# Performance work log

Measured on AMD Instinct MI355X. Metric: run time of the kernel, lower is better.

The kernel has to match this reference:

```python
import jax, jax.numpy as jnp
import numpy as np

IN_DIM, DIM, H, L, B, N = 20, 128, 8, 3, 2, 192
DH = DIM // H
EPS = 1e-5


def _conv1d(x, w):
    # x: [b, Cin, n], w: [Cout, Cin, 3], pad=1
    return jax.lax.conv_general_dilated(x, w, (1,), [(1, 1)], dimension_numbers=('NCH', 'OIH', 'NCH'))


def _conv2d(x, w):
    # x: [b, Cin, n, n], w: [Cout, Cin, 3, 3], pad=1
    return jax.lax.conv_general_dilated(x, w, (1, 1), [(1, 1), (1, 1)], dimension_numbers=('NCHW', 'OIHW', 'NCHW'))


def _bn(x, g, b, axes):
    # BatchNorm in training mode (batch statistics, biased variance), channel axis = 1
    m = jnp.mean(x, axes, keepdims=True)
    v = jnp.var(x, axes, keepdims=True)
    sh = [1] * x.ndim
    sh[1] = -1
    return (x - m) / jnp.sqrt(v + EPS) * g.reshape(sh) + b.reshape(sh)


def _ln(x, g, b):
    m = jnp.mean(x, -1, keepdims=True)
    v = jnp.var(x, -1, keepdims=True)
    return (x - m) / jnp.sqrt(v + EPS) * g + b


def _seq2pair(c):
    # c: [b, C, n] -> [b, 2C, n, n]; first C channels constant over j, second C constant over i
    b, C, n = c.shape
    a = jnp.broadcast_to(c[:, :, :, None], (b, C, n, n))
    p = jnp.broadcast_to(c[:, :, None, :], (b, C, n, n))
    return jnp.concatenate([a, p], axis=1)


def _forward(seq, mask, conv1_w, conv2_w, ln_g, ln_b, c1d_w, bn1_g, bn1_b, c2d_w, bn2_g, bn2_b,
             wq_w, wq_b, wk_w, wk_b, wv_w, wv_b, wd_w, wd_b, wl_w, wl_b, fc_w, fc_b):
    b, n, _ = seq.shape
    s = seq.transpose(0, 2, 1)                    # [b, in_dim, n]
    x = _conv1d(s, conv1_w).transpose(0, 2, 1)    # [b, n, dim]
    c = _conv1d(s, conv2_w)                       # [b, dim, n]
    c2 = _seq2pair(c)                             # [b, 2*dim, n, n]
    scale = jnp.sqrt(jnp.asarray(DH, x.dtype))
    m4 = mask[:, None, None, :]                   # [b, 1, 1, n]
    for i in range(L):
        c = jax.nn.relu(_bn(_conv1d(c, c1d_w[i]), bn1_g[i], bn1_b[i], (0, 2)))
        x = _ln(x + c.transpose(0, 2, 1), ln_g[i], ln_b[i])
        c2 = c2 + _seq2pair(c)
        c2 = jax.nn.relu(_bn(_conv2d(c2, c2d_w[i]), bn2_g[i], bn2_b[i], (0, 2, 3)))
        dsym = c2 + c2.transpose(0, 1, 3, 2)      # symmetric pair features [b, 2*dim, n, n]
        gate = jax.nn.sigmoid(jnp.einsum('bcij,hc->bhij', dsym, wd_w[i]) + wd_b[i][None, :, None, None])
        heads = lambda y: y.reshape(b, n, H, DH).transpose(0, 2, 1, 3)
        q = heads(jax.nn.relu(x @ wq_w[i].T + wq_b[i]))
        k = heads(jax.nn.relu(x @ wk_w[i].T + wk_b[i]))
        v = heads(jax.nn.relu(x @ wv_w[i].T + wv_b[i]))
        a = jnp.einsum('bhid,bhjd->bhij', q, k) / scale
        e = jnp.exp(a - jnp.max(a, -1, keepdims=True)) * m4   # hand-rolled masked softmax
        attn = e / (jnp.sum(e, -1, keepdims=True) + 1e-6)
        attn = attn * gate                        # post-softmax multiplicative pair bias
        upd = jnp.einsum('bhij,bhjd->bhid', attn, v).transpose(0, 2, 1, 3).reshape(b, n, DIM)
        x = jax.nn.relu((x + upd) @ wl_w[i].T + wl_b[i])   # dropout = identity (eval)
    return jax.nn.relu(x @ fc_w.T + fc_b)


def setup_inputs():
    key = jax.random.key(0)
    ks = jax.random.split(key, 16)
    rn = lambda k, shape, s=0.05: jax.random.normal(k, shape, jnp.float32) * s
    C2 = 2 * DIM
    return {
        'seq': jax.random.normal(ks[0], (B, N, IN_DIM), jnp.float32),
        'mask': (jax.random.uniform(ks[1], (B, N)) > 0.1).astype(jnp.float32),
        'conv1_w': rn(ks[2], (DIM, IN_DIM, 3)),
        'conv2_w': rn(ks[3], (DIM, IN_DIM, 3)),
        'ln_g': jnp.ones((L, DIM), jnp.float32),
        'ln_b': jnp.zeros((L, DIM), jnp.float32),
        'c1d_w': rn(ks[4], (L, DIM, DIM, 3)),
        'bn1_g': jnp.ones((L, DIM), jnp.float32),
        'bn1_b': jnp.zeros((L, DIM), jnp.float32),
        'c2d_w': rn(ks[5], (L, C2, C2, 3, 3), 0.02),
        'bn2_g': jnp.ones((L, C2), jnp.float32),
        'bn2_b': jnp.zeros((L, C2), jnp.float32),
        'wq_w': rn(ks[6], (L, DIM, DIM)), 'wq_b': jnp.zeros((L, DIM), jnp.float32),
        'wk_w': rn(ks[7], (L, DIM, DIM)), 'wk_b': jnp.zeros((L, DIM), jnp.float32),
        'wv_w': rn(ks[8], (L, DIM, DIM)), 'wv_b': jnp.zeros((L, DIM), jnp.float32),
        'wd_w': rn(ks[9], (L, H, C2)), 'wd_b': jnp.zeros((L, H), jnp.float32),
        'wl_w': rn(ks[10], (L, DIM, DIM)), 'wl_b': jnp.zeros((L, DIM), jnp.float32),
        'fc_w': rn(ks[11], (DIM, DIM)), 'fc_b': jnp.zeros((DIM,), jnp.float32),
    }


def reference(seq, mask, conv1_w, conv2_w, ln_g, ln_b, c1d_w, bn1_g, bn1_b, c2d_w, bn2_g, bn2_b,
              wq_w, wq_b, wk_w, wk_b, wv_w, wv_b, wd_w, wd_b, wl_w, wl_b, fc_w, fc_b):
    return _forward(seq, mask, conv1_w, conv2_w, ln_g, ln_b, c1d_w, bn1_g, bn1_b, c2d_w, bn2_g, bn2_b,
                    wq_w, wq_b, wk_w, wk_b, wv_w, wv_b, wd_w, wd_b, wl_w, wl_b, fc_w, fc_b)
```

## Files before the change

kernel.cpp:

```cpp
#include <hip/hip_runtime.h>
#include <math.h>

#define IN_DIM 20
#define DIM 128
#define HH 8
#define LL 3
#define BB 2
#define NP 192
#define DHH 16
#define C2 256
#define NN (NP*NP)
#define EPS 1e-5f

#define PR 200
#define PC 224

typedef __bf16 bf16x8 __attribute__((ext_vector_type(8)));
typedef float  f32x16 __attribute__((ext_vector_type(16)));

union Pack8 { __bf16 h[8]; uint4 u; };

#define GLOAD16(gp, lp) \
  __builtin_amdgcn_global_load_lds((const __attribute__((address_space(1))) uint4*)(gp), \
                                   (__attribute__((address_space(3))) uint4*)(lp), 16, 0, 0)

__global__ void k_conv_init(const float* __restrict__ seq, const float* __restrict__ w1,
                            const float* __restrict__ w2, float* __restrict__ X,
                            float* __restrict__ Cc) {
  int t = blockIdx.x, b = blockIdx.y, oc = threadIdx.x;
  __shared__ float ss[3][IN_DIM];
  if (threadIdx.x < 3*IN_DIM) {
    int k = threadIdx.x / IN_DIM, ic = threadIdx.x % IN_DIM;
    int tt = t + k - 1;
    ss[k][ic] = (tt >= 0 && tt < NP) ? seq[(b*NP + tt)*IN_DIM + ic] : 0.f;
  }
  __syncthreads();
  float a1 = 0.f, a2 = 0.f;
  #pragma unroll
  for (int ic = 0; ic < IN_DIM; ic++) {
    #pragma unroll
    for (int k = 0; k < 3; k++) {
      float sv = ss[k][ic];
      a1 = fmaf(w1[(oc*IN_DIM + ic)*3 + k], sv, a1);
      a2 = fmaf(w2[(oc*IN_DIM + ic)*3 + k], sv, a2);
    }
  }
  X[(b*NP + t)*DIM + oc] = a1;
  Cc[(b*DIM + oc)*NP + t] = a2;
}

__global__ void k_conv1d_bn_relu(const float* __restrict__ cin, const float* __restrict__ w,
                                 const float* __restrict__ g, const float* __restrict__ bb,
                                 float* __restrict__ cout) {
  int oc = blockIdx.x;
  int t = threadIdx.x;
  float raw[BB];
  for (int b = 0; b < BB; b++) {
    float acc = 0.f;
    for (int ic = 0; ic < DIM; ic++) {
      const float* cr = cin + (b*DIM + ic)*NP;
      const float* wr = w + (oc*DIM + ic)*3;
      float lf = (t > 0)      ? cr[t-1] : 0.f;
      float mf = cr[t];
      float rf = (t < NP-1)   ? cr[t+1] : 0.f;
      acc = fmaf(lf, wr[0], acc);
      acc = fmaf(mf, wr[1], acc);
      acc = fmaf(rf, wr[2], acc);
    }
    raw[b] = acc;
  }
  __shared__ float sb[NP];
  sb[t] = raw[0] + raw[1];
  __syncthreads();
  for (int s = 128; s > 0; s >>= 1) {
    if (t < s && t + s < NP) sb[t] += sb[t + s];
    __syncthreads();
  }
  float mean = sb[0] / (float)(BB*NP);
  __syncthreads();
  sb[t] = raw[0]*raw[0] + raw[1]*raw[1];
  __syncthreads();
  for (int s = 128; s > 0; s >>= 1) {
    if (t < s && t + s < NP) sb[t] += sb[t + s];
    __syncthreads();
  }
  float var = sb[0] / (float)(BB*NP) - mean*mean;
  float rstd = rsqrtf(var + EPS);
  float gg = g[oc], bo = bb[oc];
  for (int b = 0; b < BB; b++)
    cout[(b*DIM + oc)*NP + t] = fmaxf((raw[b] - mean)*rstd*gg + bo, 0.f);
}

__global__ void k_wtrans(const float* __restrict__ wq, const float* __restrict__ wk,
                         const float* __restrict__ wv, const float* __restrict__ wl,
                         const float* __restrict__ fcw,
                         float* __restrict__ wqt, float* __restrict__ wkt,
                         float* __restrict__ wvt, float* __restrict__ wlt,
                         float* __restrict__ fct) {
  int m = blockIdx.y;
  const float* src; float* dst;
  if (m < 3)       { src = wq + (size_t)m*DIM*DIM;     dst = wqt + (size_t)m*DIM*DIM; }
  else if (m < 6)  { src = wk + (size_t)(m-3)*DIM*DIM; dst = wkt + (size_t)(m-3)*DIM*DIM; }
  else if (m < 9)  { src = wv + (size_t)(m-6)*DIM*DIM; dst = wvt + (size_t)(m-6)*DIM*DIM; }
  else if (m < 12) { src = wl + (size_t)(m-9)*DIM*DIM; dst = wlt + (size_t)(m-9)*DIM*DIM; }
  else             { src = fcw;                        dst = fct; }
  int tile = blockIdx.x;
  int ti = tile >> 2, tj = tile & 3;
  int r = threadIdx.x >> 3, c4 = threadIdx.x & 7;
  __shared__ float t[32][33];
  float4 v = *(const float4*)(src + (ti*32 + r)*DIM + tj*32 + c4*4);
  t[r][c4*4+0] = v.x; t[r][c4*4+1] = v.y; t[r][c4*4+2] = v.z; t[r][c4*4+3] = v.w;
  __syncthreads();
  float4 o;
  o.x = t[c4*4+0][r]; o.y = t[c4*4+1][r]; o.z = t[c4*4+2][r]; o.w = t[c4*4+3][r];
  *(float4*)(dst + (tj*32 + r)*DIM + ti*32 + c4*4) = o;
}

__global__ void k_lnqkv(float* __restrict__ X, const float* __restrict__ cc,
                        const float* __restrict__ g, const float* __restrict__ bb,
                        const float* __restrict__ wqt, const float* __restrict__ bq,
                        const float* __restrict__ wkt, const float* __restrict__ bk,
                        const float* __restrict__ wvt, const float* __restrict__ bv,
                        float* __restrict__ Q, float* __restrict__ K, float* __restrict__ V) {
  int t = blockIdx.x, b = blockIdx.y, d = threadIdx.x;
  __shared__ float sb[DIM];
  __shared__ float sy[DIM];
  float v = X[(b*NP + t)*DIM + d] + cc[(b*DIM + d)*NP + t];
  sb[d] = v; __syncthreads();
  for (int s = 64; s > 0; s >>= 1) { if (d < s) sb[d] += sb[d+s]; __syncthreads(); }
  float mean = sb[0] / (float)DIM;
  __syncthreads();
  float dv = v - mean;
  sb[d] = dv*dv; __syncthreads();
  for (int s = 64; s > 0; s >>= 1) { if (d < s) sb[d] += sb[d+s]; __syncthreads(); }
  float var = sb[0] / (float)DIM;
  float rstd = rsqrtf(var + EPS);
  float xn = dv * rstd * g[d] + bb[d];
  X[(b*NP + t)*DIM + d] = xn;
  sy[d] = xn;
  __syncthreads();
  float aq = bq[d], ak = bk[d], av = bv[d];
  for (int e = 0; e < DIM; e++) {
    float xv = sy[e];
    aq = fmaf(wqt[e*DIM + d], xv, aq);
    ak = fmaf(wkt[e*DIM + d], xv, ak);
    av = fmaf(wvt[e*DIM + d], xv, av);
  }
  int h = d >> 4, dh = d & 15;
  size_t o = ((size_t)(b*HH + h)*NP + t)*DHH + dh;
  Q[o] = fmaxf(aq, 0.f); K[o] = fmaxf(ak, 0.f); V[o] = fmaxf(av, 0.f);
}

__global__ void k_wprep(const float* __restrict__ w, __bf16* __restrict__ wtb) {
  int l = blockIdx.x / C2, oc = blockIdx.x % C2;
  int tid = threadIdx.x;
  __shared__ float swt[C2*9];
  const float4* wsrc = (const float4*)(w + ((size_t)(l*C2 + oc))*C2*9);
  for (int idx = tid; idx < 576; idx += 256) ((float4*)swt)[idx] = wsrc[idx];
  __syncthreads();
  for (int v = tid; v < 288; v += 256) {
    int chunk = v / 18, rem = v % 18;
    int kk = rem >> 1, kh = rem & 1;
    Pack8 p;
    #pragma unroll
    for (int e = 0; e < 8; e++)
      p.h[e] = (__bf16)swt[(chunk*16 + kh*8 + e)*9 + kk];
    size_t unit = ((((size_t)(l*16 + chunk)*9 + kk)*2 + kh)*256 + oc);
    ((uint4*)wtb)[unit] = p.u;
  }
}

__global__ void k_make_convin(const float* __restrict__ Cc, const float* __restrict__ CL0,
                              __bf16* __restrict__ inb, float* __restrict__ STATALL) {
  int idx = blockIdx.x*256 + threadIdx.x;
  if (blockIdx.x == 0) {
    for (int z = threadIdx.x; z < 3*2*C2; z += 256) STATALL[z] = 0.f;
  }
  int kh = idx & 1;
  int t = idx >> 1;
  int gcol = t % PC; int t2 = t / PC;
  int grow = t2 % PR; int t3 = t2 / PR;
  int chunk = t3 & 15; int b = t3 >> 4;
  int i = grow - 1, j = gcol - 8;
  Pack8 p;
  if ((unsigned)i < 192u && (unsigned)j < 192u) {
    #pragma unroll
    for (int e = 0; e < 8; e++) {
      int c = chunk*16 + kh*8 + e;
      float v;
      if (c < DIM) v = Cc[(b*DIM + c)*NP + i] + CL0[(b*DIM + c)*NP + i];
      else { int cc = c - DIM; v = Cc[(b*DIM + cc)*NP + j] + CL0[(b*DIM + cc)*NP + j]; }
      p.h[e] = (__bf16)v;
    }
  } else {
    #pragma unroll
    for (int e = 0; e < 8; e++) p.h[e] = (__bf16)0.f;
  }
  ((uint4*)inb)[idx] = p.u;
}

__global__ __launch_bounds__(256, 2)
void k_conv2d_mfma(const __bf16* __restrict__ inb,
                   const __bf16* __restrict__ wtb,
                   __bf16* __restrict__ rawb,
                   float* __restrict__ STAT2) {
  __shared__ __align__(16) uint4 sbuf[2*2176];
  int tid = threadIdx.x;
  int jt = blockIdx.x, it = blockIdx.y, zz = blockIdx.z;
  int b = zz >> 3, oct = zz & 7;
  int i0 = it*8, j0 = jt*64, oc0 = oct*32;
  int lane = tid & 63, wv = tid >> 6;
  int ln31 = lane & 31, khl = lane >> 5;

  const uint4* gW = (const uint4*)wtb;
  const uint4* gI = (const uint4*)inb;

  f32x16 acc[2][2];
  #pragma unroll
  for (int r = 0; r < 2; r++)
    #pragma unroll
    for (int n = 0; n < 2; n++)
      #pragma unroll
      for (int q = 0; q < 16; q++) acc[r][n][q] = 0.f;

  const uint4* gp[9];
  int lofs[9];
  int gstride[9];
  bool gvalid[9];
  #pragma unroll
  for (int t = 0; t < 9; t++) {
    int L = t*4 + wv;
    gvalid[t] = (L < 34);
    if (L < 9) {
      int u = L*64 + lane;
      int kkh = u >> 5;
      int ocl = u & 31;
      gp[t] = gW + (size_t)kkh*256 + oc0 + ocl;
      lofs[t] = u;
      gstride[t] = 4608;
    } else {
      int u = L*64 + lane - 576;
      int r = u / 160;
      int rem = u % 160;
      int kh = rem / 80;
      int c = rem % 80;
      gp[t] = gI + (((size_t)(b*16)*PR) + i0 + r)*PC*2 + (size_t)(j0 + c)*2 + kh;
      lofs[t] = 576 + u;
      gstride[t] = PR*PC*2;
    }
  }

  auto issue = [&](int buf) {
    uint4* lbase = sbuf + buf*2176;
    #pragma unroll
    for (int t = 0; t < 9; t++) {
      if (gvalid[t]) {
        GLOAD16(gp[t], lbase + lofs[t]);
        gp[t] += gstride[t];
      }
    }
  };

  issue(0);

  for (int chunk = 0; chunk < 16; ++chunk) {
    int buf = chunk & 1;
    __syncthreads();
    if (chunk < 15) issue(buf ^ 1);
    const __bf16* Wl = (const __bf16*)(sbuf + buf*2176);
    const __bf16* Il = (const __bf16*)(sbuf + buf*2176 + 576);
    #pragma unroll
    for (int kj = 0; kj < 3; kj++) {
      bf16x8 bfr[4][2];
      #pragma unroll
      for (int rr = 0; rr < 4; rr++) {
        int r = wv*2 + rr;
        #pragma unroll
        for (int ch = 0; ch < 2; ch++) {
          int c = ch*32 + ln31 + kj + 7;
          bfr[rr][ch] = *(const bf16x8*)(Il + ((r*2 + khl)*80 + c)*8);
        }
      }
      #pragma unroll
      for (int ki = 0; ki < 3; ki++) {
        int kk = ki*3 + kj;
        bf16x8 a = *(const bf16x8*)(Wl + ((kk*2 + khl)*32 + ln31)*8);
        #pragma unroll
        for (int row = 0; row < 2; row++)
          #pragma unroll
          for (int ch = 0; ch < 2; ch++)
            acc[row][ch] = __builtin_amdgcn_mfma_f32_32x32x16_bf16(a, bfr[row + ki][ch], acc[row][ch], 0, 0, 0);
      }
    }
  }

  __syncthreads();
  float* trAll = (float*)sbuf;
  float* tr = trAll + wv*(32*33);
  float* sstat = trAll + 4*32*33;
  if (tid < 64) sstat[tid] = 0.f;
  __syncthreads();

  #pragma unroll
  for (int reg = 0; reg < 16; reg++) {
    float v00 = acc[0][0][reg], v01 = acc[0][1][reg];
    float v10 = acc[1][0][reg], v11 = acc[1][1][reg];
    float s = v00 + v01 + v10 + v11;
    float s2 = v00*v00 + v01*v01 + v10*v10 + v11*v11;
    #pragma unroll
    for (int msk = 1; msk <= 16; msk <<= 1) { s += __shfl_xor(s, msk); s2 += __shfl_xor(s2, msk); }
    if (ln31 == 0) {
      int oc_l = (reg & 3) + 8*(reg >> 2) + 4*khl;
      atomicAdd(&sstat[oc_l], s);
      atomicAdd(&sstat[32 + oc_l], s2);
    }
  }

  int Gb = oc0 >> 3;
  uint4* RAWu = (uint4*)rawb;
  #pragma unroll
  for (int row = 0; row < 2; row++) {
    int i = i0 + wv*2 + row;
    #pragma unroll
    for (int ch = 0; ch < 2; ch++) {
      #pragma unroll
      for (int reg = 0; reg < 16; reg++) {
        int r = (reg & 3) + 8*(reg >> 2) + 4*khl;
        tr[r*33 + ln31] = acc[row][ch][reg];
      }
      __builtin_amdgcn_s_waitcnt(0);
      #pragma unroll
      for (int gs = 0; gs < 2; gs++) {
        int g = khl + gs*2;
        Pack8 p;
        #pragma unroll
        for (int e = 0; e < 8; e++) p.h[e] = (__bf16)tr[(g*8 + e)*33 + ln31];
        RAWu[((size_t)(b*32 + Gb + g)*192 + i)*192 + j0 + ch*32 + ln31] = p.u;
      }
      __builtin_amdgcn_s_waitcnt(0);
    }
  }

  __syncthreads();
  if (tid < 32) {
    atomicAdd(&STAT2[oc0 + tid], sstat[tid]);
    atomicAdd(&STAT2[C2 + oc0 + tid], sstat[32 + tid]);
  }
}

template<int WRITE_NEXT>
__global__ void k_bn2_norm_gate(const __bf16* __restrict__ rawb, const float* __restrict__ STAT2,
                                const float* __restrict__ g, const float* __restrict__ bb,
                                const float* __restrict__ wd, const float* __restrict__ CLn,
                                __bf16* __restrict__ inb_next, float* __restrict__ tg) {
  int i = blockIdx.x, b = blockIdx.y, j = threadIdx.x;
  __shared__ float sscale[C2], sshift[C2], swd[HH*C2];
  const float inv = 1.f / (float)(BB*NN);
  for (int c = j; c < C2; c += 192) {
    float mean = STAT2[c] * inv;
    float var  = STAT2[C2 + c] * inv - mean*mean;
    float rstd = rsqrtf(var + EPS);
    float sc = rstd * g[c];
    sscale[c] = sc;
    sshift[c] = bb[c] - mean*sc;
  }
  for (int idx = j; idx < HH*C2; idx += 192) swd[idx] = wd[idx];
  __syncthreads();
  float gacc[HH] = {};
  const uint4* RAWu = (const uint4*)rawb;
  for (int cu = 0; cu < 32; cu++) {
    Pack8 pr; pr.u = RAWu[((size_t)(b*32 + cu)*NP + i)*NP + j];
    Pack8 p;
    #pragma unroll
    for (int e = 0; e < 8; e++) {
      int c = cu*8 + e;
      float v = (float)pr.h[e];
      v = fmaxf(fmaf(v, sscale[c], sshift[c]), 0.f);
      if (WRITE_NEXT) {
        float nv = v + ((c < DIM) ? CLn[(b*DIM + c)*NP + i] : CLn[(b*DIM + c - DIM)*NP + j]);
        p.h[e] = (__bf16)nv;
      }
      #pragma unroll
      for (int h = 0; h < HH; h++) gacc[h] = fmaf(v, swd[h*C2 + c], gacc[h]);
    }
    if (WRITE_NEXT) {
      size_t unit = ((((size_t)(b*16 + (cu>>1))*PR + (i+1))*PC + (j+8))*2 + (cu&1));
      ((uint4*)inb_next)[unit] = p.u;
    }
  }
  for (int h = 0; h < HH; h++)
    tg[((size_t)(b*HH + h)*NP + i)*NP + j] = gacc[h];
}

__global__ void k_gate(const float* __restrict__ tg, const float* __restrict__ wdb,
                       float* __restrict__ gate) {
  int tile = blockIdx.x;
  int hb = blockIdx.y;
  int b = hb >> 3, h = hb & 7;
  size_t bh = (size_t)(b*HH + h);
  int ti = tile / 6, tj = tile % 6;
  int r = threadIdx.x >> 3, c4 = threadIdx.x & 7;
  __shared__ float tB[32][33];
  const float* base = tg + bh*NN;
  float4 vb = *(const float4*)(base + (tj*32 + r)*NP + ti*32 + c4*4);
  tB[r][c4*4+0] = vb.x; tB[r][c4*4+1] = vb.y; tB[r][c4*4+2] = vb.z; tB[r][c4*4+3] = vb.w;
  __syncthreads();
  float4 va = *(const float4*)(base + (ti*32 + r)*NP + tj*32 + c4*4);
  float bias = wdb[h];
  float4 o;
  o.x = 1.f / (1.f + expf(-(va.x + tB[c4*4+0][r] + bias)));
  o.y = 1.f / (1.f + expf(-(va.y + tB[c4*4+1][r] + bias)));
  o.z = 1.f / (1.f + expf(-(va.z + tB[c4*4+2][r] + bias)));
  o.w = 1.f / (1.f + expf(-(va.w + tB[c4*4+3][r] + bias)));
  *(float4*)(gate + bh*NN + (ti*32 + r)*NP + tj*32 + c4*4) = o;
}

template<int MODE>
__global__ __launch_bounds__(192)
void k_attnx(const float* __restrict__ Q, const float* __restrict__ K,
             const float* __restrict__ V, const float* __restrict__ gate,
             const float* __restrict__ mask,
             float* __restrict__ X,
             const float* __restrict__ wlt, const float* __restrict__ bl,
             const float* __restrict__ ccn,
             const float* __restrict__ lng, const float* __restrict__ lnb,
             const float* __restrict__ wqt, const float* __restrict__ bq,
             const float* __restrict__ wkt, const float* __restrict__ bk,
             const float* __restrict__ wvt, const float* __restrict__ bv,
             float* __restrict__ Qn, float* __restrict__ Kn, float* __restrict__ Vn,
             const float* __restrict__ fct, const float* __restrict__ fb,
             float* __restrict__ out) {
  int i = blockIdx.x, b = blockIdx.y, j = threadIdx.x;
  int lane = j & 63, wvv = j >> 6;
  __shared__ float sq[DIM];
  __shared__ float sattn[HH][NP];
  __shared__ float supd[DIM];
  __shared__ float sy[DIM];
  __shared__ float sredm[HH][3];
  __shared__ float sreds[HH][3];
  __shared__ float sred[3];
  float mk = mask[b*NP + j];

  if (j < DIM) {
    int h = j >> 4, d = j & 15;
    sq[j] = Q[(((size_t)(b*HH + h))*NP + i)*DHH + d];
  }
  __syncthreads();

  float a[HH], gt[HH];
  #pragma unroll
  for (int h = 0; h < HH; h++) {
    size_t bh = (size_t)(b*HH + h);
    const float4* kr = (const float4*)(K + (bh*NP + j)*DHH);
    const float4* qr = (const float4*)(sq + h*DHH);
    float acc = 0.f;
    #pragma unroll
    for (int q4 = 0; q4 < 4; q4++) {
      float4 qv = qr[q4], kv = kr[q4];
      acc = fmaf(qv.x, kv.x, acc); acc = fmaf(qv.y, kv.y, acc);
      acc = fmaf(qv.z, kv.z, acc); acc = fmaf(qv.w, kv.w, acc);
    }
    a[h] = acc * 0.25f;
    gt[h] = gate[(bh*NP + i)*NP + j];
  }
  #pragma unroll
  for (int h = 0; h < HH; h++) {
    float m = a[h];
    #pragma unroll
    for (int s = 32; s > 0; s >>= 1) m = fmaxf(m, __shfl_xor(m, s));
    if (lane == 0) sredm[h][wvv] = m;
  }
  __syncthreads();
  float e[HH];
  #pragma unroll
  for (int h = 0; h < HH; h++) {
    float amax = fmaxf(fmaxf(sredm[h][0], sredm[h][1]), sredm[h][2]);
    e[h] = expf(a[h] - amax) * mk;
    float ss = e[h];
    #pragma unroll
    for (int s = 32; s > 0; s >>= 1) ss += __shfl_xor(ss, s);
    if (lane == 0) sreds[h][wvv] = ss;
  }
  __syncthreads();
  #pragma unroll
  for (int h = 0; h < HH; h++) {
    float denom = sreds[h][0] + sreds[h][1] + sreds[h][2] + 1e-6f;
    sattn[h][j] = (e[h] / denom) * gt[h];
  }
  __syncthreads();

  if (j < DIM) {
    int h = j >> 4, d = j & 15;
    size_t bh = (size_t)(b*HH + h);
    float acc = 0.f;
    for (int jj = 0; jj < NP; jj++)
      acc = fmaf(sattn[h][jj], V[(bh*NP + jj)*DHH + d], acc);
    supd[h*DHH + d] = acc;
  }
  __syncthreads();

  size_t o = (size_t)(b*NP + i)*DIM;
  if (j < DIM) sy[j] = X[o + j] + supd[j];
  __syncthreads();
  float xr = 0.f;
  if (j < DIM) {
    float acc = bl[j];
    for (int ee = 0; ee < DIM; ee++) acc = fmaf(wlt[ee*DIM + j], sy[ee], acc);
    xr = fmaxf(acc, 0.f);
  }
  __syncthreads();

  if (MODE == 0) {
    float v = 0.f;
    if (j < DIM) v = xr + ccn[(b*DIM + j)*NP + i];
    float s = (j < DIM) ? v : 0.f;
    #pragma unroll
    for (int m = 32; m > 0; m >>= 1) s += __shfl_xor(s, m);
    if (lane == 0 && wvv < 2) sred[wvv] = s;
    __syncthreads();
    float mean = (sred[0] + sred[1]) * (1.f/128.f);
    float dv = v - mean;
    float q = (j < DIM) ? dv*dv : 0.f;
    #pragma unroll
    for (int m = 32; m > 0; m >>= 1) q += __shfl_xor(q, m);
    __syncthreads();
    if (lane == 0 && wvv < 2) sred[wvv] = q;
    __syncthreads();
    float var = (sred[0] + sred[1]) * (1.f/128.f);
    float rstd = rsqrtf(var + EPS);
    if (j < DIM) {
      float xn = dv * rstd * lng[j] + lnb[j];
      X[o + j] = xn;
      sy[j] = xn;
    }
    __syncthreads();
    if (j < DIM) {
      float aq = bq[j], ak = bk[j], av = bv[j];
      for (int ee = 0; ee < DIM; ee++) {
        float xv = sy[ee];
        aq = fmaf(wqt[ee*DIM + j], xv, aq);
        ak = fmaf(wkt[ee*DIM + j], xv, ak);
        av = fmaf(wvt[ee*DIM + j], xv, av);
      }
      int h = j >> 4, dh = j & 15;
      size_t oo = ((size_t)(b*HH + h)*NP + i)*DHH + dh;
      Qn[oo] = fmaxf(aq, 0.f); Kn[oo] = fmaxf(ak, 0.f); Vn[oo] = fmaxf(av, 0.f);
    }
  } else {
    if (j < DIM) sy[j] = xr;
    __syncthreads();
    if (j < DIM) {
      float acc = fb[j];
      for (int ee = 0; ee < DIM; ee++) acc = fmaf(fct[ee*DIM + j], sy[ee], acc);
      out[o + j] = fmaxf(acc, 0.f);
    }
  }
}

extern "C" void kernel_launch(void* const* d_in, const int* in_sizes, int n_in,
                              void* d_out, int out_size, void* d_ws, size_t ws_size,
                              hipStream_t stream) {
  const float* seq     = (const float*)d_in[0];
  const float* mask    = (const float*)d_in[1];
  const float* conv1_w = (const float*)d_in[2];
  const float* conv2_w = (const float*)d_in[3];
  const float* ln_g    = (const float*)d_in[4];
  const float* ln_b    = (const float*)d_in[5];
  const float* c1d_w   = (const float*)d_in[6];
  const float* bn1_g   = (const float*)d_in[7];
  const float* bn1_b   = (const float*)d_in[8];
  const float* c2d_w   = (const float*)d_in[9];
  const float* bn2_g   = (const float*)d_in[10];
  const float* bn2_b   = (const float*)d_in[11];
  const float* wq_w    = (const float*)d_in[12];
  const float* wq_b    = (const float*)d_in[13];
  const float* wk_w    = (const float*)d_in[14];
  const float* wk_b    = (const float*)d_in[15];
  const float* wv_w    = (const float*)d_in[16];
  const float* wv_b    = (const float*)d_in[17];
  const float* wd_w    = (const float*)d_in[18];
  const float* wd_b    = (const float*)d_in[19];
  const float* wl_w    = (const float*)d_in[20];
  const float* wl_b    = (const float*)d_in[21];
  const float* fc_w    = (const float*)d_in[22];
  const float* fc_b    = (const float*)d_in[23];
  float* out = (float*)d_out;

  float* ws = (float*)d_ws;
  float* X    = ws; ws += BB*NP*DIM;
  float* Cc   = ws; ws += BB*DIM*NP;
  float* CL0  = ws; ws += BB*DIM*NP;
  float* CL1  = ws; ws += BB*DIM*NP;
  float* CL2  = ws; ws += BB*DIM*NP;
  float* Q0   = ws; ws += BB*NP*DIM;
  float* K0   = ws; ws += BB*NP*DIM;
  float* V0   = ws; ws += BB*NP*DIM;
  float* Q1   = ws; ws += BB*NP*DIM;
  float* K1   = ws; ws += BB*NP*DIM;
  float* V1   = ws; ws += BB*NP*DIM;
  float* TG   = ws; ws += (size_t)BB*HH*NN;
  float* GATE = ws; ws += (size_t)BB*HH*NN;
  float* WQT  = ws; ws += (size_t)LL*DIM*DIM;
  float* WKT  = ws; ws += (size_t)LL*DIM*DIM;
  float* WVT  = ws; ws += (size_t)LL*DIM*DIM;
  float* WLT  = ws; ws += (size_t)LL*DIM*DIM;
  float* FCT  = ws; ws += (size_t)DIM*DIM;
  float* STATALL = ws; ws += 3*2*C2;
  __bf16* RAW = (__bf16*)ws; ws += (size_t)BB*C2*NN/2;
  __bf16* INB = (__bf16*)ws; ws += (size_t)BB*16*PR*PC*2*16/4;
  __bf16* WTB = (__bf16*)ws; ws += (size_t)LL*C2*C2*9/2;

  k_wtrans<<<dim3(16, 13), 256, 0, stream>>>(wq_w, wk_w, wv_w, wl_w, fc_w,
                                             WQT, WKT, WVT, WLT, FCT);
  k_wprep<<<LL*C2, 256, 0, stream>>>(c2d_w, WTB);
  k_conv_init<<<dim3(NP, BB), DIM, 0, stream>>>(seq, conv1_w, conv2_w, X, Cc);
  k_conv1d_bn_relu<<<DIM, NP, 0, stream>>>(Cc,  c1d_w + 0*(size_t)DIM*DIM*3, bn1_g + 0*DIM, bn1_b + 0*DIM, CL0);
  k_conv1d_bn_relu<<<DIM, NP, 0, stream>>>(CL0, c1d_w + 1*(size_t)DIM*DIM*3, bn1_g + 1*DIM, bn1_b + 1*DIM, CL1);
  k_conv1d_bn_relu<<<DIM, NP, 0, stream>>>(CL1, c1d_w + 2*(size_t)DIM*DIM*3, bn1_g + 2*DIM, bn1_b + 2*DIM, CL2);
  k_make_convin<<<(BB*16*PR*PC*2)/256, 256, 0, stream>>>(Cc, CL0, INB, STATALL);
  k_lnqkv<<<dim3(NP, BB), DIM, 0, stream>>>(X, CL0, ln_g, ln_b,
                                            WQT, wq_b, WKT, wk_b, WVT, wv_b, Q0, K0, V0);

  k_conv2d_mfma<<<dim3(3, 24, 16), 256, 0, stream>>>(INB, WTB + 0*(size_t)16*9*2*256*8, RAW, STATALL + 0*2*C2);
  k_bn2_norm_gate<1><<<dim3(NP, BB), NP, 0, stream>>>(RAW, STATALL + 0*2*C2, bn2_g + 0*C2, bn2_b + 0*C2,
                                                      wd_w + 0*(size_t)HH*C2, CL1, INB, TG);
  k_gate<<<dim3(36, 16), 256, 0, stream>>>(TG, wd_b + 0*HH, GATE);
  k_attnx<0><<<dim3(NP, BB), NP, 0, stream>>>(Q0, K0, V0, GATE, mask, X,
                                              WLT + 0*(size_t)DIM*DIM, wl_b + 0*DIM,
                                              CL1, ln_g + 1*DIM, ln_b + 1*DIM,
                                              WQT + 1*(size_t)DIM*DIM, wq_b + 1*DIM,
                                              WKT + 1*(size_t)DIM*DIM, wk_b + 1*DIM,
                                              WVT + 1*(size_t)DIM*DIM, wv_b + 1*DIM,
                                              Q1, K1, V1, nullptr, nullptr, nullptr);
  k_conv2d_mfma<<<dim3(3, 24, 16), 256, 0, stream>>>(INB, WTB + 1*(size_t)16*9*2*256*8, RAW, STATALL + 1*2*C2);
  k_bn2_norm_gate<1><<<dim3(NP, BB), NP, 0, stream>>>(RAW, STATALL + 1*2*C2, bn2_g + 1*C2, bn2_b + 1*C2,
                                                      wd_w + 1*(size_t)HH*C2, CL2, INB, TG);
  k_gate<<<dim3(36, 16), 256, 0, stream>>>(TG, wd_b + 1*HH, GATE);
  k_attnx<0><<<dim3(NP, BB), NP, 0, stream>>>(Q1, K1, V1, GATE, mask, X,
                                              WLT + 1*(size_t)DIM*DIM, wl_b + 1*DIM,
                                              CL2, ln_g + 2*DIM, ln_b + 2*DIM,
                                              WQT + 2*(size_t)DIM*DIM, wq_b + 2*DIM,
                                              WKT + 2*(size_t)DIM*DIM, wk_b + 2*DIM,
                                              WVT + 2*(size_t)DIM*DIM, wv_b + 2*DIM,
                                              Q0, K0, V0, nullptr, nullptr, nullptr);
  k_conv2d_mfma<<<dim3(3, 24, 16), 256, 0, stream>>>(INB, WTB + 2*(size_t)16*9*2*256*8, RAW, STATALL + 2*2*C2);
  k_bn2_norm_gate<0><<<dim3(NP, BB), NP, 0, stream>>>(RAW, STATALL + 2*2*C2, bn2_g + 2*C2, bn2_b + 2*C2,
                                                      wd_w + 2*(size_t)HH*C2, nullptr, nullptr, TG);
  k_gate<<<dim3(36, 16), 256, 0, stream>>>(TG, wd_b + 2*HH, GATE);
  k_attnx<1><<<dim3(NP, BB), NP, 0, stream>>>(Q0, K0, V0, GATE, mask, X,
                                              WLT + 2*(size_t)DIM*DIM, wl_b + 2*DIM,
                                              nullptr, nullptr, nullptr,
                                              nullptr, nullptr, nullptr, nullptr, nullptr, nullptr,
                                              nullptr, nullptr, nullptr,
                                              FCT, fc_b, out);
}
```

Baseline: 680.1 us.

## Split per-thread work across more threads in conv1d, bn2-gate and attention kernels

Raises block sizes for three small kernels and splits each thread's serial loops. The 1-D conv gets 768 threads (batch × input-channel halves) with a merged mean/variance reduction. The BN2+gate pass splits its channel loop in half and combines through shared memory. The attention kernel splits heads, PV sums and the linear layers across 384 threads. The aim is to cut the long serial dependency chains and idle lanes in these latency-bound kernels, at the cost of extra shared-memory reductions and barriers.

```diff
diff --git a/kernel.cpp b/kernel.cpp
--- a/kernel.cpp
+++ b/kernel.cpp
@@ -49,46 +49,44 @@
   Cc[(b*DIM + oc)*NP + t] = a2;
 }
 
-__global__ void k_conv1d_bn_relu(const float* __restrict__ cin, const float* __restrict__ w,
-                                 const float* __restrict__ g, const float* __restrict__ bb,
-                                 float* __restrict__ cout) {
+__global__ __launch_bounds__(768)
+void k_conv1d_bn_relu(const float* __restrict__ cin, const float* __restrict__ w,
+                      const float* __restrict__ g, const float* __restrict__ bb,
+                      float* __restrict__ cout) {
   int oc = blockIdx.x;
-  int t = threadIdx.x;
-  float raw[BB];
-  for (int b = 0; b < BB; b++) {
-    float acc = 0.f;
-    for (int ic = 0; ic < DIM; ic++) {
-      const float* cr = cin + (b*DIM + ic)*NP;
-      const float* wr = w + (oc*DIM + ic)*3;
-      float lf = (t > 0)      ? cr[t-1] : 0.f;
-      float mf = cr[t];
-      float rf = (t < NP-1)   ? cr[t+1] : 0.f;
-      acc = fmaf(lf, wr[0], acc);
-      acc = fmaf(mf, wr[1], acc);
-      acc = fmaf(rf, wr[2], acc);
-    }
-    raw[b] = acc;
-  }
-  __shared__ float sb[NP];
-  sb[t] = raw[0] + raw[1];
-  __syncthreads();
-  for (int s = 128; s > 0; s >>= 1) {
-    if (t < s && t + s < NP) sb[t] += sb[t + s];
+  int tid = threadIdx.x;
+  int t = tid % NP;
+  int sub = tid / NP;
+  int b = sub & 1, ih = sub >> 1;
+  float acc = 0.f;
+  for (int ic = ih*64; ic < ih*64 + 64; ic++) {
+    const float* cr = cin + (b*DIM + ic)*NP;
+    const float* wr = w + (oc*DIM + ic)*3;
+    float lf = (t > 0)      ? cr[t-1] : 0.f;
+    float mf = cr[t];
+    float rf = (t < NP-1)   ? cr[t+1] : 0.f;
+    acc = fmaf(lf, wr[0], acc);
+    acc = fmaf(mf, wr[1], acc);
+    acc = fmaf(rf, wr[2], acc);
+  }
+  __shared__ float sp[4][NP];
+  __shared__ float sb[768];
+  sp[sub][t] = acc;
+  __syncthreads();
+  float raw = sp[b][t] + sp[2 + b][t];
+  sb[tid] = (sub < 2) ? raw : raw * raw;
+  __syncthreads();
+  for (int s = 192; s >= 3; s >>= 1) {
+    if (tid < s) sb[tid] += sb[tid + s];
+    int u = tid - 384;
+    if (u >= 0 && u < s) sb[tid] += sb[tid + s];
     __syncthreads();
   }
-  float mean = sb[0] / (float)(BB*NP);
-  __syncthreads();
-  sb[t] = raw[0]*raw[0] + raw[1]*raw[1];
-  __syncthreads();
-  for (int s = 128; s > 0; s >>= 1) {
-    if (t < s && t + s < NP) sb[t] += sb[t + s];
-    __syncthreads();
-  }
-  float var = sb[0] / (float)(BB*NP) - mean*mean;
+  float mean = (sb[0] + sb[1] + sb[2]) / 384.f;
+  float var  = (sb[384] + sb[385] + sb[386]) / 384.f - mean*mean;
   float rstd = rsqrtf(var + EPS);
-  float gg = g[oc], bo = bb[oc];
-  for (int b = 0; b < BB; b++)
-    cout[(b*DIM + oc)*NP + t] = fmaxf((raw[b] - mean)*rstd*gg + bo, 0.f);
+  if (sub < 2)
+    cout[(b*DIM + oc)*NP + t] = fmaxf((raw - mean)*rstd*g[oc] + bb[oc], 0.f);
 }
 
 __global__ void k_wtrans(const float* __restrict__ wq, const float* __restrict__ wk,
@@ -349,14 +347,18 @@
 }
 
 template<int WRITE_NEXT>
-__global__ void k_bn2_norm_gate(const __bf16* __restrict__ rawb, const float* __restrict__ STAT2,
-                                const float* __restrict__ g, const float* __restrict__ bb,
-                                const float* __restrict__ wd, const float* __restrict__ CLn,
-                                __bf16* __restrict__ inb_next, float* __restrict__ tg) {
-  int i = blockIdx.x, b = blockIdx.y, j = threadIdx.x;
+__global__ __launch_bounds__(384)
+void k_bn2_norm_gate(const __bf16* __restrict__ rawb, const float* __restrict__ STAT2,
+                     const float* __restrict__ g, const float* __restrict__ bb,
+                     const float* __restrict__ wd, const float* __restrict__ CLn,
+                     __bf16* __restrict__ inb_next, float* __restrict__ tg) {
+  int i = blockIdx.x, b = blockIdx.y;
+  int tid = threadIdx.x;
+  int j = tid % 192, half = tid / 192;
   __shared__ float sscale[C2], sshift[C2], swd[HH*C2];
+  __shared__ float sg[2][HH][192];
   const float inv = 1.f / (float)(BB*NN);
-  for (int c = j; c < C2; c += 192) {
+  for (int c = tid; c < C2; c += 384) {
     float mean = STAT2[c] * inv;
     float var  = STAT2[C2 + c] * inv - mean*mean;
     float rstd = rsqrtf(var + EPS);
@@ -364,11 +366,11 @@
     sscale[c] = sc;
     sshift[c] = bb[c] - mean*sc;
   }
-  for (int idx = j; idx < HH*C2; idx += 192) swd[idx] = wd[idx];
+  for (int idx = tid; idx < HH*C2; idx += 384) swd[idx] = wd[idx];
   __syncthreads();
   float gacc[HH] = {};
   const uint4* RAWu = (const uint4*)rawb;
-  for (int cu = 0; cu < 32; cu++) {
+  for (int cu = half*16; cu < half*16 + 16; cu++) {
     Pack8 pr; pr.u = RAWu[((size_t)(b*32 + cu)*NP + i)*NP + j];
     Pack8 p;
     #pragma unroll
@@ -388,8 +390,14 @@
       ((uint4*)inb_next)[unit] = p.u;
     }
   }
-  for (int h = 0; h < HH; h++)
-    tg[((size_t)(b*HH + h)*NP + i)*NP + j] = gacc[h];
+  #pragma unroll
+  for (int h = 0; h < HH; h++) sg[half][h][j] = gacc[h];
+  __syncthreads();
+  if (half == 0) {
+    #pragma unroll
+    for (int h = 0; h < HH; h++)
+      tg[((size_t)(b*HH + h)*NP + i)*NP + j] = sg[0][h][j] + sg[1][h][j];
+  }
 }
 
 __global__ void k_gate(const float* __restrict__ tg, const float* __restrict__ wdb,
@@ -416,7 +424,7 @@
 }
 
 template<int MODE>
-__global__ __launch_bounds__(192)
+__global__ __launch_bounds__(384)
 void k_attnx(const float* __restrict__ Q, const float* __restrict__ K,
              const float* __restrict__ V, const float* __restrict__ gate,
              const float* __restrict__ mask,
@@ -430,26 +438,31 @@
              float* __restrict__ Qn, float* __restrict__ Kn, float* __restrict__ Vn,
              const float* __restrict__ fct, const float* __restrict__ fb,
              float* __restrict__ out) {
-  int i = blockIdx.x, b = blockIdx.y, j = threadIdx.x;
-  int lane = j & 63, wvv = j >> 6;
+  int i = blockIdx.x, b = blockIdx.y;
+  int tid = threadIdx.x;
+  int j = tid % 192, half = tid / 192;
+  int lane = tid & 63, wave = tid >> 6;
   __shared__ float sq[DIM];
   __shared__ float sattn[HH][NP];
+  __shared__ float spv[3][DIM];
   __shared__ float supd[DIM];
   __shared__ float sy[DIM];
+  __shared__ float sxp[3][DIM];
   __shared__ float sredm[HH][3];
   __shared__ float sreds[HH][3];
-  __shared__ float sred[3];
+  __shared__ float sred[2];
   float mk = mask[b*NP + j];
 
-  if (j < DIM) {
-    int h = j >> 4, d = j & 15;
-    sq[j] = Q[(((size_t)(b*HH + h))*NP + i)*DHH + d];
-  }
-  __syncthreads();
-
-  float a[HH], gt[HH];
-  #pragma unroll
-  for (int h = 0; h < HH; h++) {
+  if (tid < DIM) {
+    int h = tid >> 4, d = tid & 15;
+    sq[tid] = Q[(((size_t)(b*HH + h))*NP + i)*DHH + d];
+  }
+  __syncthreads();
+
+  float a[4], gt[4];
+  #pragma unroll
+  for (int hh = 0; hh < 4; hh++) {
+    int h = half*4 + hh;
     size_t bh = (size_t)(b*HH + h);
     const float4* kr = (const float4*)(K + (bh*NP + j)*DHH);
     const float4* qr = (const float4*)(sq + h*DHH);
@@ -460,100 +473,115 @@
       acc = fmaf(qv.x, kv.x, acc); acc = fmaf(qv.y, kv.y, acc);
       acc = fmaf(qv.z, kv.z, acc); acc = fmaf(qv.w, kv.w, acc);
     }
-    a[h] = acc * 0.25f;
-    gt[h] = gate[(bh*NP + i)*NP + j];
-  }
-  #pragma unroll
-  for (int h = 0; h < HH; h++) {
-    float m = a[h];
+    a[hh] = acc * 0.25f;
+    gt[hh] = gate[(bh*NP + i)*NP + j];
+  }
+  #pragma unroll
+  for (int hh = 0; hh < 4; hh++) {
+    int h = half*4 + hh;
+    float m = a[hh];
     #pragma unroll
     for (int s = 32; s > 0; s >>= 1) m = fmaxf(m, __shfl_xor(m, s));
-    if (lane == 0) sredm[h][wvv] = m;
-  }
-  __syncthreads();
-  float e[HH];
-  #pragma unroll
-  for (int h = 0; h < HH; h++) {
+    if (lane == 0) sredm[h][wave % 3] = m;
+  }
+  __syncthreads();
+  float e[4];
+  #pragma unroll
+  for (int hh = 0; hh < 4; hh++) {
+    int h = half*4 + hh;
     float amax = fmaxf(fmaxf(sredm[h][0], sredm[h][1]), sredm[h][2]);
-    e[h] = expf(a[h] - amax) * mk;
-    float ss = e[h];
+    e[hh] = expf(a[hh] - amax) * mk;
+    float ss = e[hh];
     #pragma unroll
     for (int s = 32; s > 0; s >>= 1) ss += __shfl_xor(ss, s);
-    if (lane == 0) sreds[h][wvv] = ss;
-  }
-  __syncthreads();
-  #pragma unroll
-  for (int h = 0; h < HH; h++) {
+    if (lane == 0) sreds[h][wave % 3] = ss;
+  }
+  __syncthreads();
+  #pragma unroll
+  for (int hh = 0; hh < 4; hh++) {
+    int h = half*4 + hh;
     float denom = sreds[h][0] + sreds[h][1] + sreds[h][2] + 1e-6f;
-    sattn[h][j] = (e[h] / denom) * gt[h];
-  }
-  __syncthreads();
-
-  if (j < DIM) {
-    int h = j >> 4, d = j & 15;
-    size_t bh = (size_t)(b*HH + h);
+    sattn[h][j] = (e[hh] / denom) * gt[hh];
+  }
+  __syncthreads();
+
+  {
+    int d = tid & 15, h2 = (tid >> 4) & 7, jseg = tid >> 7;
+    size_t bh = (size_t)(b*HH + h2);
     float acc = 0.f;
-    for (int jj = 0; jj < NP; jj++)
-      acc = fmaf(sattn[h][jj], V[(bh*NP + jj)*DHH + d], acc);
-    supd[h*DHH + d] = acc;
-  }
+    for (int jj = jseg*64; jj < jseg*64 + 64; jj++)
+      acc = fmaf(sattn[h2][jj], V[(bh*NP + jj)*DHH + d], acc);
+    spv[jseg][h2*DHH + d] = acc;
+  }
+  __syncthreads();
+  if (tid < DIM) supd[tid] = spv[0][tid] + spv[1][tid] + spv[2][tid];
   __syncthreads();
 
   size_t o = (size_t)(b*NP + i)*DIM;
-  if (j < DIM) sy[j] = X[o + j] + supd[j];
+  if (tid < DIM) sy[tid] = X[o + tid] + supd[tid];
+  __syncthreads();
+  {
+    int d2 = tid & 127, ks = tid >> 7;
+    int e0 = ks*43, e1 = (ks == 2) ? 128 : e0 + 43;
+    float acc = (ks == 0) ? bl[d2] : 0.f;
+    for (int ee = e0; ee < e1; ee++) acc = fmaf(wlt[ee*DIM + d2], sy[ee], acc);
+    sxp[ks][d2] = acc;
+  }
   __syncthreads();
   float xr = 0.f;
-  if (j < DIM) {
-    float acc = bl[j];
-    for (int ee = 0; ee < DIM; ee++) acc = fmaf(wlt[ee*DIM + j], sy[ee], acc);
-    xr = fmaxf(acc, 0.f);
-  }
+  if (tid < DIM) xr = fmaxf(sxp[0][tid] + sxp[1][tid] + sxp[2][tid], 0.f);
   __syncthreads();
 
   if (MODE == 0) {
     float v = 0.f;
-    if (j < DIM) v = xr + ccn[(b*DIM + j)*NP + i];
-    float s = (j < DIM) ? v : 0.f;
-    #pragma unroll
-    for (int m = 32; m > 0; m >>= 1) s += __shfl_xor(s, m);
-    if (lane == 0 && wvv < 2) sred[wvv] = s;
+    if (tid < DIM) v = xr + ccn[(b*DIM + tid)*NP + i];
+    if (tid < DIM) {
+      float s = v;
+      #pragma unroll
+      for (int m = 32; m > 0; m >>= 1) s += __shfl_xor(s, m);
+      if (lane == 0) sred[wave] = s;
+    }
     __syncthreads();
     float mean = (sred[0] + sred[1]) * (1.f/128.f);
     float dv = v - mean;
-    float q = (j < DIM) ? dv*dv : 0.f;
-    #pragma unroll
-    for (int m = 32; m > 0; m >>= 1) q += __shfl_xor(q, m);
-    __syncthreads();
-    if (lane == 0 && wvv < 2) sred[wvv] = q;
+    if (tid < DIM) {
+      float q = dv*dv;
+      #pragma unroll
+      for (int m = 32; m > 0; m >>= 1) q += __shfl_xor(q, m);
+      if (lane == 0) sred[wave] = q;
+    }
     __syncthreads();
     float var = (sred[0] + sred[1]) * (1.f/128.f);
     float rstd = rsqrtf(var + EPS);
-    if (j < DIM) {
-      float xn = dv * rstd * lng[j] + lnb[j];
-      X[o + j] = xn;
-      sy[j] = xn;
+    if (tid < DIM) {
+      float xn = dv * rstd * lng[tid] + lnb[tid];
+      X[o + tid] = xn;
+      sy[tid] = xn;
     }
     __syncthreads();
-    if (j < DIM) {
-      float aq = bq[j], ak = bk[j], av = bv[j];
-      for (int ee = 0; ee < DIM; ee++) {
-        float xv = sy[ee];
-        aq = fmaf(wqt[ee*DIM + j], xv, aq);
-        ak = fmaf(wkt[ee*DIM + j], xv, ak);
-        av = fmaf(wvt[ee*DIM + j], xv, av);
-      }
-      int h = j >> 4, dh = j & 15;
-      size_t oo = ((size_t)(b*HH + h)*NP + i)*DHH + dh;
-      Qn[oo] = fmaxf(aq, 0.f); Kn[oo] = fmaxf(ak, 0.f); Vn[oo] = fmaxf(av, 0.f);
+    {
+      int d2 = tid & 127, m = tid >> 7;
+      const float* wt_m = (m == 0) ? wqt : (m == 1) ? wkt : wvt;
+      const float* b_m  = (m == 0) ? bq  : (m == 1) ? bk  : bv;
+      float* out_m      = (m == 0) ? Qn  : (m == 1) ? Kn  : Vn;
+      float acc = b_m[d2];
+      for (int ee = 0; ee < DIM; ee++) acc = fmaf(wt_m[ee*DIM + d2], sy[ee], acc);
+      int h = d2 >> 4, dh = d2 & 15;
+      out_m[((size_t)(b*HH + h)*NP + i)*DHH + dh] = fmaxf(acc, 0.f);
     }
   } else {
-    if (j < DIM) sy[j] = xr;
+    if (tid < DIM) sy[tid] = xr;
     __syncthreads();
-    if (j < DIM) {
-      float acc = fb[j];
-      for (int ee = 0; ee < DIM; ee++) acc = fmaf(fct[ee*DIM + j], sy[ee], acc);
-      out[o + j] = fmaxf(acc, 0.f);
-    }
+    {
+      int d2 = tid & 127, ks = tid >> 7;
+      int e0 = ks*43, e1 = (ks == 2) ? 128 : e0 + 43;
+      float acc = (ks == 0) ? fb[d2] : 0.f;
+      for (int ee = e0; ee < e1; ee++) acc = fmaf(fct[ee*DIM + d2], sy[ee], acc);
+      sxp[ks][d2] = acc;
+    }
+    __syncthreads();
+    if (tid < DIM)
+      out[o + tid] = fmaxf(sxp[0][tid] + sxp[1][tid] + sxp[2][tid], 0.f);
   }
 }
 
@@ -614,43 +642,43 @@
                                              WQT, WKT, WVT, WLT, FCT);
   k_wprep<<<LL*C2, 256, 0, stream>>>(c2d_w, WTB);
   k_conv_init<<<dim3(NP, BB), DIM, 0, stream>>>(seq, conv1_w, conv2_w, X, Cc);
-  k_conv1d_bn_relu<<<DIM, NP, 0, stream>>>(Cc,  c1d_w + 0*(size_t)DIM*DIM*3, bn1_g + 0*DIM, bn1_b + 0*DIM, CL0);
-  k_conv1d_bn_relu<<<DIM, NP, 0, stream>>>(CL0, c1d_w + 1*(size_t)DIM*DIM*3, bn1_g + 1*DIM, bn1_b + 1*DIM, CL1);
-  k_conv1d_bn_relu<<<DIM, NP, 0, stream>>>(CL1, c1d_w + 2*(size_t)DIM*DIM*3, bn1_g + 2*DIM, bn1_b + 2*DIM, CL2);
+  k_conv1d_bn_relu<<<DIM, 768, 0, stream>>>(Cc,  c1d_w + 0*(size_t)DIM*DIM*3, bn1_g + 0*DIM, bn1_b + 0*DIM, CL0);
+  k_conv1d_bn_relu<<<DIM, 768, 0, stream>>>(CL0, c1d_w + 1*(size_t)DIM*DIM*3, bn1_g + 1*DIM, bn1_b + 1*DIM, CL1);
+  k_conv1d_bn_relu<<<DIM, 768, 0, stream>>>(CL1, c1d_w + 2*(size_t)DIM*DIM*3, bn1_g + 2*DIM, bn1_b + 2*DIM, CL2);
   k_make_convin<<<(BB*16*PR*PC*2)/256, 256, 0, stream>>>(Cc, CL0, INB, STATALL);
   k_lnqkv<<<dim3(NP, BB), DIM, 0, stream>>>(X, CL0, ln_g, ln_b,
                                             WQT, wq_b, WKT, wk_b, WVT, wv_b, Q0, K0, V0);
 
   k_conv2d_mfma<<<dim3(3, 24, 16), 256, 0, stream>>>(INB, WTB + 0*(size_t)16*9*2*256*8, RAW, STATALL + 0*2*C2);
-  k_bn2_norm_gate<1><<<dim3(NP, BB), NP, 0, stream>>>(RAW, STATALL + 0*2*C2, bn2_g + 0*C2, bn2_b + 0*C2,
-                                                      wd_w + 0*(size_t)HH*C2, CL1, INB, TG);
+  k_bn2_norm_gate<1><<<dim3(NP, BB), 384, 0, stream>>>(RAW, STATALL + 0*2*C2, bn2_g + 0*C2, bn2_b + 0*C2,
+                                                       wd_w + 0*(size_t)HH*C2, CL1, INB, TG);
   k_gate<<<dim3(36, 16), 256, 0, stream>>>(TG, wd_b + 0*HH, GATE);
-  k_attnx<0><<<dim3(NP, BB), NP, 0, stream>>>(Q0, K0, V0, GATE, mask, X,
-                                              WLT + 0*(size_t)DIM*DIM, wl_b + 0*DIM,
-                                              CL1, ln_g + 1*DIM, ln_b + 1*DIM,
-                                              WQT + 1*(size_t)DIM*DIM, wq_b + 1*DIM,
-                                              WKT + 1*(size_t)DIM*DIM, wk_b + 1*DIM,
-                                              WVT + 1*(size_t)DIM*DIM, wv_b + 1*DIM,
-                                              Q1, K1, V1, nullptr, nullptr, nullptr);
+  k_attnx<0><<<dim3(NP, BB), 384, 0, stream>>>(Q0, K0, V0, GATE, mask, X,
+                                               WLT + 0*(size_t)DIM*DIM, wl_b + 0*DIM,
+                                               CL1, ln_g + 1*DIM, ln_b + 1*DIM,
+                                               WQT + 1*(size_t)DIM*DIM, wq_b + 1*DIM,
+                                               WKT + 1*(size_t)DIM*DIM, wk_b + 1*DIM,
+                                               WVT + 1*(size_t)DIM*DIM, wv_b + 1*DIM,
+                                               Q1, K1, V1, nullptr, nullptr, nullptr);
   k_conv2d_mfma<<<dim3(3, 24, 16), 256, 0, stream>>>(INB, WTB + 1*(size_t)16*9*2*256*8, RAW, STATALL + 1*2*C2);
-  k_bn2_norm_gate<1><<<dim3(NP, BB), NP, 0, stream>>>(RAW, STATALL + 1*2*C2, bn2_g + 1*C2, bn2_b + 1*C2,
-                                                      wd_w + 1*(size_t)HH*C2, CL2, INB, TG);
+  k_bn2_norm_gate<1><<<dim3(NP, BB), 384, 0, stream>>>(RAW, STATALL + 1*2*C2, bn2_g + 1*C2, bn2_b + 1*C2,
+                                                       wd_w + 1*(size_t)HH*C2, CL2, INB, TG);
   k_gate<<<dim3(36, 16), 256, 0, stream>>>(TG, wd_b + 1*HH, GATE);
-  k_attnx<0><<<dim3(NP, BB), NP, 0, stream>>>(Q1, K1, V1, GATE, mask, X,
-                                              WLT + 1*(size_t)DIM*DIM, wl_b + 1*DIM,
-                                              CL2, ln_g + 2*DIM, ln_b + 2*DIM,
-                                              WQT + 2*(size_t)DIM*DIM, wq_b + 2*DIM,
-                                              WKT + 2*(size_t)DIM*DIM, wk_b + 2*DIM,
-                                              WVT + 2*(size_t)DIM*DIM, wv_b + 2*DIM,
-                                              Q0, K0, V0, nullptr, nullptr, nullptr);
+  k_attnx<0><<<dim3(NP, BB), 384, 0, stream>>>(Q1, K1, V1, GATE, mask, X,
+                                               WLT + 1*(size_t)DIM*DIM, wl_b + 1*DIM,
+                                               CL2, ln_g + 2*DIM, ln_b + 2*DIM,
+                                               WQT + 2*(size_t)DIM*DIM, wq_b + 2*DIM,
+                                               WKT + 2*(size_t)DIM*DIM, wk_b + 2*DIM,
+                                               WVT + 2*(size_t)DIM*DIM, wv_b + 2*DIM,
+                                               Q0, K0, V0, nullptr, nullptr, nullptr);
   k_conv2d_mfma<<<dim3(3, 24, 16), 256, 0, stream>>>(INB, WTB + 2*(size_t)16*9*2*256*8, RAW, STATALL + 2*2*C2);
-  k_bn2_norm_gate<0><<<dim3(NP, BB), NP, 0, stream>>>(RAW, STATALL + 2*2*C2, bn2_g + 2*C2, bn2_b + 2*C2,
-                                                      wd_w + 2*(size_t)HH*C2, nullptr, nullptr, TG);
+  k_bn2_norm_gate<0><<<dim3(NP, BB), 384, 0, stream>>>(RAW, STATALL + 2*2*C2, bn2_g + 2*C2, bn2_b + 2*C2,
+                                                       wd_w + 2*(size_t)HH*C2, nullptr, nullptr, TG);
   k_gate<<<dim3(36, 16), 256, 0, stream>>>(TG, wd_b + 2*HH, GATE);
-  k_attnx<1><<<dim3(NP, BB), NP, 0, stream>>>(Q0, K0, V0, GATE, mask, X,
-                                              WLT + 2*(size_t)DIM*DIM, wl_b + 2*DIM,
-                                              nullptr, nullptr, nullptr,
-                                              nullptr, nullptr, nullptr, nullptr, nullptr, nullptr,
-                                              nullptr, nullptr, nullptr,
-                                              FCT, fc_b, out);
-}
+  k_attnx<1><<<dim3(NP, BB), 384, 0, stream>>>(Q0, K0, V0, GATE, mask, X,
+                                               WLT + 2*(size_t)DIM*DIM, wl_b + 2*DIM,
+                                               nullptr, nullptr, nullptr,
+                                               nullptr, nullptr, nullptr, nullptr, nullptr, nullptr,
+                                               nullptr, nullptr, nullptr,
+                                               FCT, fc_b, out);
+}
```

Measured after the change: 591.5 us. 1.15x faster.
